# Optimization experiments

Hardware: AMD Instinct MI355X
Metric: run time of the kernel (lower is better)

## Reference

```python
import jax, jax.numpy as jnp
import numpy as np

DIM = 512
HEADS = 8
EPS = 1e-5


def layer_norm(x, g, b):
    mu = jnp.mean(x, axis=-1, keepdims=True)
    var = jnp.mean(jnp.square(x - mu), axis=-1, keepdims=True)
    return (x - mu) * jax.lax.rsqrt(var + EPS) * g + b


def setup_inputs() -> dict:
    key = jax.random.key(0)
    ks = jax.random.split(key, 8)
    d = DIM
    s = 0.02
    return {
        "x": jax.random.normal(ks[0], (2, d, 64, 64), jnp.float32),
        "ln1_g": jnp.ones((d,), jnp.float32),
        "ln1_b": jnp.zeros((d,), jnp.float32),
        "w_qkv": jax.random.normal(ks[1], (d, 3 * d), jnp.float32) * s,
        "b_qkv": jnp.zeros((3 * d,), jnp.float32),
        "w_proj": jax.random.normal(ks[2], (d, d), jnp.float32) * s,
        "b_proj": jnp.zeros((d,), jnp.float32),
        "ln2_g": jnp.ones((d,), jnp.float32),
        "ln2_b": jnp.zeros((d,), jnp.float32),
        "w_ffn1": jax.random.normal(ks[3], (d, 4 * d), jnp.float32) * s,
        "b_ffn1": jnp.zeros((4 * d,), jnp.float32),
        "w_ffn2": jax.random.normal(ks[4], (4 * d, d), jnp.float32) * s,
        "b_ffn2": jnp.zeros((d,), jnp.float32),
    }


def reference(x, ln1_g, ln1_b, w_qkv, b_qkv, w_proj, b_proj,
              ln2_g, ln2_b, w_ffn1, b_ffn1, w_ffn2, b_ffn2):
    B, C, H, W = x.shape
    hd = C // HEADS
    x_in = x
    t = x.reshape(B, C, H * W).transpose(0, 2, 1)  # [B, N, C]
    h = layer_norm(t, ln1_g, ln1_b)
    qkv = h @ w_qkv + b_qkv  # [B, N, 3C]
    q, k, v = jnp.split(qkv, 3, axis=-1)
    def to_heads(a):
        return a.reshape(B, -1, HEADS, hd).transpose(0, 2, 1, 3)  # [B, h, N, hd]
    q, k, v = to_heads(q), to_heads(k), to_heads(v)
    # NOTE: module scales by 1/sqrt(C), not 1/sqrt(head_dim)
    attn = jnp.einsum('bhqd,bhkd->bhqk', q, k) / jnp.sqrt(jnp.float32(C))
    attn = jax.nn.softmax(attn, axis=-1)
    out = jnp.einsum('bhqk,bhkd->bhqd', attn, v)
    out = out.transpose(0, 2, 1, 3).reshape(B, -1, C)
    out = out @ w_proj + b_proj
    t = t + out
    h2 = layer_norm(t, ln2_g, ln2_b)
    ffn = jax.nn.relu(h2 @ w_ffn1 + b_ffn1) @ w_ffn2 + b_ffn2
    t = t + ffn
    y = t.transpose(0, 2, 1).reshape(B, C, H, W)
    return y + x_in
```

## Files before the change

### kernel.cpp

```cpp
#include <hip/hip_runtime.h>
#include <hip/hip_bf16.h>

typedef __bf16 bf16;
typedef __bf16 bf16x8 __attribute__((ext_vector_type(8)));
typedef __bf16 bf16x4 __attribute__((ext_vector_type(4)));
typedef float f32x4 __attribute__((ext_vector_type(4)));
typedef int int4v __attribute__((ext_vector_type(4)));
typedef int int2v __attribute__((ext_vector_type(2)));

#define DEV static __device__ __forceinline__

DEV void gload16(const void* g, void* l) {
    __builtin_amdgcn_global_load_lds(
        (const __attribute__((address_space(1))) void*)g,
        (__attribute__((address_space(3))) void*)l, 16, 0, 0);
}

DEV f32x4 mfma16(bf16x8 a, bf16x8 b, f32x4 c) {
    return __builtin_amdgcn_mfma_f32_16x16x32_bf16(a, b, c, 0, 0, 0);
}

DEV int cvtpk(float lo, float hi) {
    int r;
    asm("v_cvt_pk_bf16_f32 %0, %1, %2" : "=v"(r) : "v"(lo), "v"(hi));
    return r;
}

DEV float rexp2(float x) {
    float r;
    asm("v_exp_f32 %0, %1" : "=v"(r) : "v"(x));
    return r;
}

__global__ __launch_bounds__(256)
void k_transpose_x(const float* __restrict__ x, float* __restrict__ t) {
    __shared__ float tile[32][33];
    int bid = blockIdx.x;
    int nt = bid & 127, ct = (bid >> 7) & 15, b = bid >> 11;
    int n0 = nt * 32, c0 = ct * 32;
    int tid = threadIdx.x;
    const float* xb = x + (size_t)b * 512 * 4096;
    int nl = tid & 31, cl = tid >> 5;
#pragma unroll
    for (int i = 0; i < 4; i++) {
        int c = cl + i * 8;
        tile[c][nl] = xb[(size_t)(c0 + c) * 4096 + n0 + nl];
    }
    __syncthreads();
    float* tb = t + (size_t)b * 4096 * 512;
    int cl2 = tid & 31, nl2 = tid >> 5;
#pragma unroll
    for (int i = 0; i < 4; i++) {
        int n = nl2 + i * 8;
        tb[(size_t)(n0 + n) * 512 + c0 + cl2] = tile[cl2][n];
    }
}

__global__ __launch_bounds__(256)
void k_out3(const float* __restrict__ t, const bf16* __restrict__ f2o,
            const float* __restrict__ x, float* __restrict__ y) {
    __shared__ float tile[32][33];
    int bid = blockIdx.x;
    int nt = bid & 127, ct = (bid >> 7) & 15, b = bid >> 11;
    int n0 = nt * 32, c0 = ct * 32;
    int tid = threadIdx.x;
#pragma unroll
    for (int i = 0; i < 4; i++) {
        int nl = (tid >> 5) + i * 8;
        size_t idx = (size_t)(b * 4096 + n0 + nl) * 512 + c0 + (tid & 31);
        tile[tid & 31][nl] = t[idx] + (float)f2o[idx];
    }
    __syncthreads();
    const float* xb = x + ((size_t)b * 512 + c0) * 4096;
    float* yb = y + ((size_t)b * 512 + c0) * 4096;
#pragma unroll
    for (int i = 0; i < 4; i++) {
        int cl = (tid >> 5) + i * 8;
        int nl = tid & 31;
        size_t off = (size_t)cl * 4096 + n0 + nl;
        yb[off] = tile[cl][nl] + xb[off];
    }
}

__global__ __launch_bounds__(256)
void k_ln(const float* __restrict__ t, const float* __restrict__ gg,
          const float* __restrict__ bb, bf16* __restrict__ h) {
    int lane = threadIdx.x & 63;
    int row = blockIdx.x * 4 + (threadIdx.x >> 6);
    const float* tr = t + (size_t)row * 512;
    f32x4 v0 = *(const f32x4*)(tr + lane * 4);
    f32x4 v1 = *(const f32x4*)(tr + 256 + lane * 4);
    float s = v0[0] + v0[1] + v0[2] + v0[3] + v1[0] + v1[1] + v1[2] + v1[3];
#pragma unroll
    for (int m = 1; m < 64; m <<= 1) s += __shfl_xor(s, m);
    float mu = s * (1.0f / 512.0f);
    float vs = 0.f;
#pragma unroll
    for (int j = 0; j < 4; j++) {
        float d0 = v0[j] - mu, d1 = v1[j] - mu;
        vs += d0 * d0 + d1 * d1;
    }
#pragma unroll
    for (int m = 1; m < 64; m <<= 1) vs += __shfl_xor(vs, m);
    float rs = rsqrtf(vs * (1.0f / 512.0f) + 1e-5f);
    f32x4 g0 = *(const f32x4*)(gg + lane * 4);
    f32x4 g1 = *(const f32x4*)(gg + 256 + lane * 4);
    f32x4 b0 = *(const f32x4*)(bb + lane * 4);
    f32x4 b1 = *(const f32x4*)(bb + 256 + lane * 4);
    bf16x4 o0, o1;
#pragma unroll
    for (int j = 0; j < 4; j++) {
        o0[j] = (bf16)((v0[j] - mu) * rs * g0[j] + b0[j]);
        o1[j] = (bf16)((v1[j] - mu) * rs * g1[j] + b1[j]);
    }
    *(bf16x4*)(h + (size_t)row * 512 + lane * 4) = o0;
    *(bf16x4*)(h + (size_t)row * 512 + 256 + lane * 4) = o1;
}

__global__ __launch_bounds__(256)
void k_lnr(float* __restrict__ t, const bf16* __restrict__ r,
           const float* __restrict__ gg, const float* __restrict__ bb,
           bf16* __restrict__ h) {
    int lane = threadIdx.x & 63;
    int row = blockIdx.x * 4 + (threadIdx.x >> 6);
    float* tr = t + (size_t)row * 512;
    f32x4 v0 = *(const f32x4*)(tr + lane * 4);
    f32x4 v1 = *(const f32x4*)(tr + 256 + lane * 4);
    bf16x4 r0 = *(const bf16x4*)(r + (size_t)row * 512 + lane * 4);
    bf16x4 r1 = *(const bf16x4*)(r + (size_t)row * 512 + 256 + lane * 4);
#pragma unroll
    for (int j = 0; j < 4; j++) {
        v0[j] += (float)r0[j];
        v1[j] += (float)r1[j];
    }
    *(f32x4*)(tr + lane * 4) = v0;
    *(f32x4*)(tr + 256 + lane * 4) = v1;
    float s = v0[0] + v0[1] + v0[2] + v0[3] + v1[0] + v1[1] + v1[2] + v1[3];
#pragma unroll
    for (int m = 1; m < 64; m <<= 1) s += __shfl_xor(s, m);
    float mu = s * (1.0f / 512.0f);
    float vs = 0.f;
#pragma unroll
    for (int j = 0; j < 4; j++) {
        float d0 = v0[j] - mu, d1 = v1[j] - mu;
        vs += d0 * d0 + d1 * d1;
    }
#pragma unroll
    for (int m = 1; m < 64; m <<= 1) vs += __shfl_xor(vs, m);
    float rs = rsqrtf(vs * (1.0f / 512.0f) + 1e-5f);
    f32x4 g0 = *(const f32x4*)(gg + lane * 4);
    f32x4 g1 = *(const f32x4*)(gg + 256 + lane * 4);
    f32x4 b0 = *(const f32x4*)(bb + lane * 4);
    f32x4 b1 = *(const f32x4*)(bb + 256 + lane * 4);
    bf16x4 o0, o1;
#pragma unroll
    for (int j = 0; j < 4; j++) {
        o0[j] = (bf16)((v0[j] - mu) * rs * g0[j] + b0[j]);
        o1[j] = (bf16)((v1[j] - mu) * rs * g1[j] + b1[j]);
    }
    *(bf16x4*)(h + (size_t)row * 512 + lane * 4) = o0;
    *(bf16x4*)(h + (size_t)row * 512 + 256 + lane * 4) = o1;
}

__global__ __launch_bounds__(256)
void k_wt(const float* __restrict__ w, bf16* __restrict__ wt, int K, int N) {
    __shared__ float tile[32][33];
    int ntn = N >> 5;
    int kt = blockIdx.x / ntn, ntile = blockIdx.x % ntn;
    int k0 = kt * 32, n0 = ntile * 32;
    int tid = threadIdx.x;
    int nl = tid & 31, kl = tid >> 5;
#pragma unroll
    for (int i = 0; i < 4; i++) {
        int k = kl + i * 8;
        tile[k][nl] = w[(size_t)(k0 + k) * N + n0 + nl];
    }
    __syncthreads();
    int kl2 = tid & 31, nl2 = tid >> 5;
#pragma unroll
    for (int i = 0; i < 4; i++) {
        int n = nl2 + i * 8;
        wt[(size_t)(n0 + n) * K + k0 + kl2] = (bf16)tile[kl2][n];
    }
}

template <int MODE, int BN>
__global__ __launch_bounds__(256, BN == 64 ? 3 : 2)
void k_gemm(const bf16* __restrict__ A, const bf16* __restrict__ BT,
            const float* __restrict__ bias, bf16* __restrict__ outb,
            bf16* __restrict__ vtout, int M, int N, int K) {
    constexpr int CG = BN / 32;
    constexpr int BSZ = CG * 4096;
    __shared__ char smem[32768 + 2 * BSZ];
    int ntn = N / BN;
    int nwg = gridDim.x;
    int bid = blockIdx.x;
    int cpx = nwg >> 3;
    bid = (bid & 7) * cpx + (bid >> 3);
    int bm = bid / ntn, bn = bid % ntn;
    int m0 = bm * 128, n0 = bn * BN;
    int tid = threadIdx.x;
    int w = tid >> 6, l = tid & 63;
    int wm = w >> 1, wn = w & 1;
    int l15 = l & 15, lg = l >> 4;

    f32x4 acc[4][CG];
#pragma unroll
    for (int i = 0; i < 4; i++)
#pragma unroll
        for (int j = 0; j < CG; j++) acc[i][j] = (f32x4){0.f, 0.f, 0.f, 0.f};

    int srow = tid >> 3, sphys = tid & 7;
    int lrow_a = wm * 64 + l15;
    int lrow_b = wn * (BN / 2) + l15;

#define GEMM_STAGE(k0v, bb)                                                  \
    do {                                                                     \
        _Pragma("unroll") for (int s = 0; s < 4; s++) {                      \
            int row = s * 32 + srow;                                         \
            int k16 = sphys ^ (row & 7);                                     \
            gload16(A + (size_t)(m0 + row) * K + (k0v) + k16 * 8,            \
                    smem + (bb) * 16384 + s * 4096 + tid * 16);              \
        }                                                                    \
        _Pragma("unroll") for (int s = 0; s < CG; s++) {                     \
            int row = s * 32 + srow;                                         \
            int k16 = sphys ^ (row & 7);                                     \
            gload16(BT + (size_t)(n0 + row) * K + (k0v) + k16 * 8,           \
                    smem + 32768 + (bb) * BSZ + s * 4096 + tid * 16);        \
        }                                                                    \
    } while (0)

    int nk = K >> 6;
    GEMM_STAGE(0, 0);
    int cur = 0;
    for (int kt = 0; kt < nk; kt++) {
        if (kt + 1 < nk) {
            GEMM_STAGE((kt + 1) << 6, cur ^ 1);
            if constexpr (BN == 128)
                asm volatile("s_waitcnt vmcnt(8)" ::: "memory");
            else
                asm volatile("s_waitcnt vmcnt(6)" ::: "memory");
        } else {
            asm volatile("s_waitcnt vmcnt(0)" ::: "memory");
        }
        __builtin_amdgcn_s_barrier();
        __builtin_amdgcn_sched_barrier(0);
        const char* pA = smem + cur * 16384;
        const char* pB = smem + 32768 + cur * BSZ;
#pragma unroll
        for (int ks = 0; ks < 2; ks++) {
            bf16x8 af[4], bfr[CG];
#pragma unroll
            for (int rg = 0; rg < 4; rg++) {
                int row = lrow_a + rg * 16;
                af[rg] = *(const bf16x8*)(pA + row * 128 +
                                          (((lg + ks * 4) ^ (row & 7)) << 4));
            }
#pragma unroll
            for (int cg = 0; cg < CG; cg++) {
                int row = lrow_b + cg * 16;
                bfr[cg] = *(const bf16x8*)(pB + row * 128 +
                                           (((lg + ks * 4) ^ (row & 7)) << 4));
            }
#pragma unroll
            for (int rg = 0; rg < 4; rg++)
#pragma unroll
                for (int cg = 0; cg < CG; cg++)
                    acc[rg][cg] = mfma16(af[rg], bfr[cg], acc[rg][cg]);
        }
        __builtin_amdgcn_s_barrier();
        cur ^= 1;
    }
#undef GEMM_STAGE

    if constexpr (MODE == 2) {
        if (n0 >= 1024) {
            char* vl = smem;
#pragma unroll
            for (int cg = 0; cg < CG; cg++) {
                int col = wn * 64 + cg * 16 + l15;
                float bz = bias[n0 + col];
#pragma unroll
                for (int rg = 0; rg < 4; rg++) {
                    int rowb = wm * 64 + rg * 16 + lg * 4;
                    int2v qq = {cvtpk(acc[rg][cg][0] + bz, acc[rg][cg][1] + bz),
                                cvtpk(acc[rg][cg][2] + bz, acc[rg][cg][3] + bz)};
                    *(int2v*)(vl + col * 272 + rowb * 2) = qq;
                }
            }
            __syncthreads();
            int b = m0 >> 12, nrow0 = m0 & 4095;
            int dl = tid >> 3, c8 = tid & 7;
#pragma unroll
            for (int dd = 0; dd < 4; dd++) {
                int d = dd * 32 + dl;
                int ch = (n0 - 1024) + d;
                bf16* dst = vtout +
                    ((size_t)((b * 8 + (ch >> 6)) * 64 + (ch & 63))) * 4096 + nrow0;
#pragma unroll
                for (int half = 0; half < 2; half++) {
                    int chunk = half * 8 + c8;
                    bf16x8 vv = *(const bf16x8*)(vl + d * 272 + chunk * 16);
                    *(bf16x8*)(dst + chunk * 8) = vv;
                }
            }
            return;
        }
    }

    constexpr int RS = BN * 2 + 8;
    constexpr int CH = BN / 8;
    char* ep = smem;
#pragma unroll
    for (int cg = 0; cg < CG; cg++) {
        int lcol = wn * (BN / 2) + cg * 16 + l15;
        float bz = bias[n0 + lcol];
#pragma unroll
        for (int rg = 0; rg < 4; rg++) {
#pragma unroll
            for (int j = 0; j < 4; j++) {
                int lrow = wm * 64 + rg * 16 + lg * 4 + j;
                float v = acc[rg][cg][j] + bz;
                if (MODE == 1) v = fmaxf(v, 0.f);
                *(bf16*)(ep + lrow * RS + lcol * 2) = (bf16)v;
            }
        }
    }
    __syncthreads();
    int cch = tid & (CH - 1);
    int rof = tid / CH;
    constexpr int RPP = 256 / CH;
#pragma unroll
    for (int i = 0; i < 128 / RPP; i++) {
        int row = i * RPP + rof;
        bf16x8 vv = *(const bf16x8*)(ep + row * RS + cch * 16);
        *(bf16x8*)(outb + (size_t)(m0 + row) * N + n0 + cch * 8) = vv;
    }
}

__global__ __launch_bounds__(256, 4)
void k_attn(const bf16* __restrict__ qkvb, const bf16* __restrict__ vt,
            bf16* __restrict__ attno) {
    __shared__ bf16 sK[2][64 * 64];
    __shared__ bf16 sV[2][64 * 64];
    const float sc = 0.044194173824159216f * 1.4426950408889634f;
    int bid = blockIdx.x;
    int nb = (bid & 7) * 128 + (bid >> 3);
    int bh = nb >> 6, qt = nb & 63;
    int b = bh >> 3, hh = bh & 7;
    int q0 = qt * 64;
    int tid = threadIdx.x, w = tid >> 6, l = tid & 63;
    int l15 = l & 15, lg = l >> 4, l7 = l15 & 7;
    int lg4 = lg * 4;
    int vperm = ((lg & 1) << 1) | (lg >> 1);
    const bf16* qbase = qkvb + (size_t)b * 4096 * 1536 + hh * 64;
    const bf16* kbase = qbase + 512;
    const bf16* vbase = vt + (size_t)bh * 64 * 4096;
    int srow = tid >> 3, sphys = tid & 7;

    const char* kp0 = (const char*)&sK[0][0] + l15 * 128 + ((lg ^ l7) << 4);
    const char* kp1 = (const char*)&sK[0][0] + l15 * 128 + (((4 + lg) ^ l7) << 4);
    const char* vp0 = (const char*)&sV[0][0] + l15 * 128 + ((vperm ^ l7) << 4);
    const char* vp1 = (const char*)&sV[0][0] + l15 * 128 + (((4 + vperm) ^ l7) << 4);
    char* dK0 = (char*)&sK[0][0] + tid * 16;
    char* dV0 = (char*)&sV[0][0] + tid * 16;
    const char* kg = (const char*)(kbase + srow * 1536 + (sphys ^ (srow & 7)) * 8);
    const char* vg = (const char*)(vbase + srow * 4096 + (sphys ^ (srow & 7)) * 8);

    gload16(kg, dK0);
    gload16(kg + 98304, dK0 + 4096);
    gload16(vg, dV0);
    gload16(vg + 262144, dV0 + 4096);
    kg += 196608;
    vg += 128;

    bf16x8 qf[2];
#pragma unroll
    for (int ks = 0; ks < 2; ks++) {
        bf16x8 v = *(const bf16x8*)(qbase +
            (size_t)(q0 + w * 16 + l15) * 1536 + ks * 32 + lg * 8);
        bf16x8 o;
#pragma unroll
        for (int j = 0; j < 8; j++) o[j] = (bf16)((float)v[j] * sc);
        qf[ks] = o;
    }

    const f32x4 kZ = {0.f, 0.f, 0.f, 0.f};
    float lsum = 0.f;
    f32x4 acc[4];
#pragma unroll
    for (int df = 0; df < 4; df++) acc[df] = kZ;

#define ABODY(BUF, PF)                                                        \
    {                                                                         \
        if (PF) {                                                             \
            gload16(kg, dK0 + (1 - (BUF)) * 8192);                            \
            gload16(kg + 98304, dK0 + (1 - (BUF)) * 8192 + 4096);             \
            gload16(vg, dV0 + (1 - (BUF)) * 8192);                            \
            gload16(vg + 262144, dV0 + (1 - (BUF)) * 8192 + 4096);            \
            kg += 196608;                                                     \
            vg += 128;                                                        \
            asm volatile("s_waitcnt vmcnt(4)" ::: "memory");                  \
        } else {                                                              \
            asm volatile("s_waitcnt vmcnt(0)" ::: "memory");                  \
        }                                                                     \
        __builtin_amdgcn_s_barrier();                                         \
        __builtin_amdgcn_sched_barrier(0);                                    \
        f32x4 s0, s1, s2, s3;                                                 \
        __builtin_amdgcn_s_setprio(1);                                        \
        s0 = mfma16(*(const bf16x8*)(kp0 + (BUF) * 8192 + 0 * 2048), qf[0], kZ); \
        s0 = mfma16(*(const bf16x8*)(kp1 + (BUF) * 8192 + 0 * 2048), qf[1], s0); \
        s1 = mfma16(*(const bf16x8*)(kp0 + (BUF) * 8192 + 1 * 2048), qf[0], kZ); \
        s1 = mfma16(*(const bf16x8*)(kp1 + (BUF) * 8192 + 1 * 2048), qf[1], s1); \
        __builtin_amdgcn_s_setprio(0);                                        \
        float e0 = rexp2(s0[0]), e1 = rexp2(s0[1]);                           \
        float e2 = rexp2(s0[2]), e3 = rexp2(s0[3]);                           \
        float e4 = rexp2(s1[0]), e5 = rexp2(s1[1]);                           \
        float e6 = rexp2(s1[2]), e7 = rexp2(s1[3]);                           \
        __builtin_amdgcn_s_setprio(1);                                        \
        s2 = mfma16(*(const bf16x8*)(kp0 + (BUF) * 8192 + 2 * 2048), qf[0], kZ); \
        s2 = mfma16(*(const bf16x8*)(kp1 + (BUF) * 8192 + 2 * 2048), qf[1], s2); \
        s3 = mfma16(*(const bf16x8*)(kp0 + (BUF) * 8192 + 3 * 2048), qf[0], kZ); \
        s3 = mfma16(*(const bf16x8*)(kp1 + (BUF) * 8192 + 3 * 2048), qf[1], s3); \
        __builtin_amdgcn_s_setprio(0);                                        \
        int p0 = cvtpk(e0, e1), p1 = cvtpk(e2, e3);                           \
        int p2 = cvtpk(e4, e5), p3 = cvtpk(e6, e7);                           \
        asm("v_permlane16_swap_b32 %0, %1" : "+v"(p2), "+v"(p0));             \
        asm("v_permlane16_swap_b32 %0, %1" : "+v"(p3), "+v"(p1));             \
        {                                                                     \
            int4v ai = {p0, p1, p2, p3};                                      \
            bf16x8 af = __builtin_bit_cast(bf16x8, ai);                       \
            __builtin_amdgcn_s_setprio(1);                                    \
            acc[0] = mfma16(af, *(const bf16x8*)(vp0 + (BUF) * 8192 + 0 * 2048), acc[0]); \
            acc[1] = mfma16(af, *(const bf16x8*)(vp0 + (BUF) * 8192 + 1 * 2048), acc[1]); \
            acc[2] = mfma16(af, *(const bf16x8*)(vp0 + (BUF) * 8192 + 2 * 2048), acc[2]); \
            acc[3] = mfma16(af, *(const bf16x8*)(vp0 + (BUF) * 8192 + 3 * 2048), acc[3]); \
            __builtin_amdgcn_s_setprio(0);                                    \
        }                                                                     \
        float e8 = rexp2(s2[0]), e9 = rexp2(s2[1]);                           \
        float e10 = rexp2(s2[2]), e11 = rexp2(s2[3]);                         \
        float e12 = rexp2(s3[0]), e13 = rexp2(s3[1]);                         \
        float e14 = rexp2(s3[2]), e15 = rexp2(s3[3]);                         \
        int p4 = cvtpk(e8, e9), p5 = cvtpk(e10, e11);                         \
        int p6 = cvtpk(e12, e13), p7 = cvtpk(e14, e15);                       \
        asm("v_permlane16_swap_b32 %0, %1" : "+v"(p6), "+v"(p4));             \
        asm("v_permlane16_swap_b32 %0, %1" : "+v"(p7), "+v"(p5));             \
        {                                                                     \
            int4v ai = {p4, p5, p6, p7};                                      \
            bf16x8 af = __builtin_bit_cast(bf16x8, ai);                       \
            __builtin_amdgcn_s_setprio(1);                                    \
            acc[0] = mfma16(af, *(const bf16x8*)(vp1 + (BUF) * 8192 + 0 * 2048), acc[0]); \
            acc[1] = mfma16(af, *(const bf16x8*)(vp1 + (BUF) * 8192 + 1 * 2048), acc[1]); \
            acc[2] = mfma16(af, *(const bf16x8*)(vp1 + (BUF) * 8192 + 2 * 2048), acc[2]); \
            acc[3] = mfma16(af, *(const bf16x8*)(vp1 + (BUF) * 8192 + 3 * 2048), acc[3]); \
            __builtin_amdgcn_s_setprio(0);                                    \
        }                                                                     \
        lsum += (((e0 + e1) + (e2 + e3)) + ((e4 + e5) + (e6 + e7))) +         \
                (((e8 + e9) + (e10 + e11)) + ((e12 + e13) + (e14 + e15)));    \
        __builtin_amdgcn_s_barrier();                                         \
    }

    for (int tt = 0; tt < 31; tt++) {
        ABODY(0, 1)
        ABODY(1, 1)
    }
    ABODY(0, 1)
    ABODY(1, 0)
#undef ABODY

    lsum += __shfl_xor(lsum, 16);
    lsum += __shfl_xor(lsum, 32);
    float invq[4];
#pragma unroll
    for (int j = 0; j < 4; j++)
        invq[j] = 1.0f / __shfl(lsum, lg4 + j);

    bf16* ow = (bf16*)&sK[0][0] + w * 16 * 64;
#pragma unroll
    for (int df = 0; df < 4; df++) {
        int chunk = df * 2 + (l15 >> 3);
        int within = l15 & 7;
#pragma unroll
        for (int j = 0; j < 4; j++) {
            int q = lg * 4 + j;
            *(bf16*)((char*)ow + q * 128 + ((chunk ^ (q & 7)) << 4) + within * 2) =
                (bf16)(acc[df][j] * invq[j]);
        }
    }
    __syncthreads();
    const char* owr = (const char*)ow;
#pragma unroll
    for (int half = 0; half < 2; half++) {
        int r = l >> 2, ch = (l & 3) + half * 4;
        bf16x8 vv = *(const bf16x8*)(owr + r * 128 + ((ch ^ (r & 7)) << 4));
        *(bf16x8*)(attno + (size_t)(b * 4096 + q0 + w * 16 + r) * 512 +
                   hh * 64 + ch * 8) = vv;
    }
}

extern "C" void kernel_launch(void* const* d_in, const int* in_sizes, int n_in,
                              void* d_out, int out_size, void* d_ws, size_t ws_size,
                              hipStream_t stream) {
    const float* x = (const float*)d_in[0];
    const float* ln1g = (const float*)d_in[1];
    const float* ln1b = (const float*)d_in[2];
    const float* wqkv = (const float*)d_in[3];
    const float* bqkv = (const float*)d_in[4];
    const float* wproj = (const float*)d_in[5];
    const float* bproj = (const float*)d_in[6];
    const float* ln2g = (const float*)d_in[7];
    const float* ln2b = (const float*)d_in[8];
    const float* wffn1 = (const float*)d_in[9];
    const float* bffn1 = (const float*)d_in[10];
    const float* wffn2 = (const float*)d_in[11];
    const float* bffn2 = (const float*)d_in[12];
    float* y = (float*)d_out;

    char* ws = (char*)d_ws;
    float* t    = (float*)(ws + 0);
    bf16* h     = (bf16*)(ws + 16777216);
    bf16* qkvb  = (bf16*)(ws + 25165824);
    bf16* vtb   = (bf16*)(ws + 50331648);
    bf16* f1    = (bf16*)(ws + 25165824);
    bf16* wqT   = (bf16*)(ws + 58720256);
    bf16* wpT   = (bf16*)(ws + 60293120);
    bf16* w1T   = (bf16*)(ws + 60817408);
    bf16* w2T   = (bf16*)(ws + 62914560);
    bf16* attno = h;
    bf16* po    = vtb;
    bf16* f2o   = h;

    k_transpose_x<<<4096, 256, 0, stream>>>(x, t);
    k_ln<<<2048, 256, 0, stream>>>(t, ln1g, ln1b, h);
    k_wt<<<(512 / 32) * (1536 / 32), 256, 0, stream>>>(wqkv, wqT, 512, 1536);
    k_wt<<<(512 / 32) * (512 / 32), 256, 0, stream>>>(wproj, wpT, 512, 512);
    k_wt<<<(512 / 32) * (2048 / 32), 256, 0, stream>>>(wffn1, w1T, 512, 2048);
    k_wt<<<(2048 / 32) * (512 / 32), 256, 0, stream>>>(wffn2, w2T, 2048, 512);

    k_gemm<2, 128><<<768, 256, 0, stream>>>(h, wqT, bqkv, qkvb, vtb, 8192, 1536, 512);
    k_attn<<<1024, 256, 0, stream>>>(qkvb, vtb, attno);
    k_gemm<0, 64><<<512, 256, 0, stream>>>(attno, wpT, bproj, po, nullptr, 8192, 512, 512);
    k_lnr<<<2048, 256, 0, stream>>>(t, po, ln2g, ln2b, h);
    k_gemm<1, 128><<<1024, 256, 0, stream>>>(h, w1T, bffn1, f1, nullptr, 8192, 2048, 512);
    k_gemm<0, 64><<<512, 256, 0, stream>>>(f1, w2T, bffn2, f2o, nullptr, 8192, 512, 2048);
    k_out3<<<4096, 256, 0, stream>>>(t, f2o, x, y);
}
```

Baseline: 201.2 us.

## Drop fp32 residual buffer, fuse transpose into layernorm, merge weight transposes

Result: no change. 204.0 us (+1.4%).

```diff
diff --git a/kernel.cpp b/kernel.cpp
--- a/kernel.cpp
+++ b/kernel.cpp
@@ -4,6 +4,7 @@
 typedef __bf16 bf16;
 typedef __bf16 bf16x8 __attribute__((ext_vector_type(8)));
 typedef __bf16 bf16x4 __attribute__((ext_vector_type(4)));
+typedef __bf16 bf16x2 __attribute__((ext_vector_type(2)));
 typedef float f32x4 __attribute__((ext_vector_type(4)));
 typedef int int4v __attribute__((ext_vector_type(4)));
 typedef int int2v __attribute__((ext_vector_type(2)));
@@ -32,141 +33,121 @@
     return r;
 }
 
-__global__ __launch_bounds__(256)
-void k_transpose_x(const float* __restrict__ x, float* __restrict__ t) {
+template <bool HASPO>
+__global__ __launch_bounds__(512)
+void k_tln(const float* __restrict__ x, const bf16* __restrict__ po,
+           const float* __restrict__ gg, const float* __restrict__ bb,
+           bf16* __restrict__ h) {
+    __shared__ bf16 big[32][520];
     __shared__ float tile[32][33];
     int bid = blockIdx.x;
-    int nt = bid & 127, ct = (bid >> 7) & 15, b = bid >> 11;
-    int n0 = nt * 32, c0 = ct * 32;
+    int nt = bid & 127, b = bid >> 7;
+    int n0 = nt * 32;
     int tid = threadIdx.x;
-    const float* xb = x + (size_t)b * 512 * 4096;
+    const float* xb = x + (size_t)b * 512 * 4096 + n0;
     int nl = tid & 31, cl = tid >> 5;
-#pragma unroll
-    for (int i = 0; i < 4; i++) {
-        int c = cl + i * 8;
-        tile[c][nl] = xb[(size_t)(c0 + c) * 4096 + n0 + nl];
+    int cl2 = tid & 31, nh = tid >> 5;
+    for (int ct = 0; ct < 16; ct++) {
+        int c0 = ct * 32;
+#pragma unroll
+        for (int i = 0; i < 2; i++) {
+            int c = cl + i * 16;
+            tile[c][nl] = xb[(size_t)(c0 + c) * 4096 + nl];
+        }
+        __syncthreads();
+#pragma unroll
+        for (int i = 0; i < 2; i++) {
+            int n = nh + i * 16;
+            big[n][c0 + cl2] = (bf16)tile[cl2][n];
+        }
+        __syncthreads();
+    }
+    int w = tid >> 6, l = tid & 63;
+    f32x4 g0 = *(const f32x4*)(gg + l * 8);
+    f32x4 g1 = *(const f32x4*)(gg + l * 8 + 4);
+    f32x4 bb0 = *(const f32x4*)(bb + l * 8);
+    f32x4 bb1 = *(const f32x4*)(bb + l * 8 + 4);
+#pragma unroll
+    for (int r = 0; r < 4; r++) {
+        int n = w * 4 + r;
+        bf16x8 vv = *(const bf16x8*)&big[n][l * 8];
+        float v[8];
+#pragma unroll
+        for (int j = 0; j < 8; j++) v[j] = (float)vv[j];
+        if (HASPO) {
+            bf16x8 pv = *(const bf16x8*)(po +
+                (size_t)(b * 4096 + n0 + n) * 512 + l * 8);
+#pragma unroll
+            for (int j = 0; j < 8; j++) v[j] += (float)pv[j];
+        }
+        float s = (((v[0] + v[1]) + (v[2] + v[3])) +
+                   ((v[4] + v[5]) + (v[6] + v[7])));
+#pragma unroll
+        for (int m = 1; m < 64; m <<= 1) s += __shfl_xor(s, m);
+        float mu = s * (1.0f / 512.0f);
+        float vs = 0.f;
+#pragma unroll
+        for (int j = 0; j < 8; j++) {
+            float d = v[j] - mu;
+            vs += d * d;
+        }
+#pragma unroll
+        for (int m = 1; m < 64; m <<= 1) vs += __shfl_xor(vs, m);
+        float rs = rsqrtf(vs * (1.0f / 512.0f) + 1e-5f);
+        bf16x8 o;
+#pragma unroll
+        for (int j = 0; j < 4; j++) {
+            o[j] = (bf16)((v[j] - mu) * rs * g0[j] + bb0[j]);
+            o[j + 4] = (bf16)((v[j + 4] - mu) * rs * g1[j] + bb1[j]);
+        }
+        *(bf16x8*)(h + (size_t)(b * 4096 + n0 + n) * 512 + l * 8) = o;
+    }
+}
+
+__global__ __launch_bounds__(256)
+void k_fin(const float* __restrict__ x, const bf16* __restrict__ po,
+           const bf16* __restrict__ f2o, float* __restrict__ y) {
+    __shared__ float ts[64][33];
+    int bid = blockIdx.x;
+    int nt = bid & 127, ct = (bid >> 7) & 7, b = bid >> 10;
+    int n0 = nt * 32, c0 = ct * 64;
+    int tid = threadIdx.x;
+    int pi = tid & 31, nr = tid >> 5;
+#pragma unroll
+    for (int p = 0; p < 4; p++) {
+        int n = nr + p * 8;
+        size_t ro = (size_t)(b * 4096 + n0 + n) * 512 + c0 + pi * 2;
+        bf16x2 pv = *(const bf16x2*)(po + ro);
+        bf16x2 fv = *(const bf16x2*)(f2o + ro);
+        ts[pi * 2][n] = (float)pv[0] + (float)fv[0];
+        ts[pi * 2 + 1][n] = (float)pv[1] + (float)fv[1];
     }
     __syncthreads();
-    float* tb = t + (size_t)b * 4096 * 512;
-    int cl2 = tid & 31, nl2 = tid >> 5;
-#pragma unroll
-    for (int i = 0; i < 4; i++) {
-        int n = nl2 + i * 8;
-        tb[(size_t)(n0 + n) * 512 + c0 + cl2] = tile[cl2][n];
+    int nw = tid & 31, cw = tid >> 5;
+#pragma unroll
+    for (int q = 0; q < 8; q++) {
+        int c = cw + q * 8;
+        size_t off = ((size_t)b * 512 + c0 + c) * 4096 + n0 + nw;
+        y[off] = 2.0f * x[off] + ts[c][nw];
     }
 }
 
 __global__ __launch_bounds__(256)
-void k_out3(const float* __restrict__ t, const bf16* __restrict__ f2o,
-            const float* __restrict__ x, float* __restrict__ y) {
+void k_wtall(const float* __restrict__ w0, const float* __restrict__ w1,
+             const float* __restrict__ w2, const float* __restrict__ w3,
+             bf16* __restrict__ d0, bf16* __restrict__ d1,
+             bf16* __restrict__ d2, bf16* __restrict__ d3) {
     __shared__ float tile[32][33];
     int bid = blockIdx.x;
-    int nt = bid & 127, ct = (bid >> 7) & 15, b = bid >> 11;
-    int n0 = nt * 32, c0 = ct * 32;
-    int tid = threadIdx.x;
-#pragma unroll
-    for (int i = 0; i < 4; i++) {
-        int nl = (tid >> 5) + i * 8;
-        size_t idx = (size_t)(b * 4096 + n0 + nl) * 512 + c0 + (tid & 31);
-        tile[tid & 31][nl] = t[idx] + (float)f2o[idx];
-    }
-    __syncthreads();
-    const float* xb = x + ((size_t)b * 512 + c0) * 4096;
-    float* yb = y + ((size_t)b * 512 + c0) * 4096;
-#pragma unroll
-    for (int i = 0; i < 4; i++) {
-        int cl = (tid >> 5) + i * 8;
-        int nl = tid & 31;
-        size_t off = (size_t)cl * 4096 + n0 + nl;
-        yb[off] = tile[cl][nl] + xb[off];
-    }
-}
-
-__global__ __launch_bounds__(256)
-void k_ln(const float* __restrict__ t, const float* __restrict__ gg,
-          const float* __restrict__ bb, bf16* __restrict__ h) {
-    int lane = threadIdx.x & 63;
-    int row = blockIdx.x * 4 + (threadIdx.x >> 6);
-    const float* tr = t + (size_t)row * 512;
-    f32x4 v0 = *(const f32x4*)(tr + lane * 4);
-    f32x4 v1 = *(const f32x4*)(tr + 256 + lane * 4);
-    float s = v0[0] + v0[1] + v0[2] + v0[3] + v1[0] + v1[1] + v1[2] + v1[3];
-#pragma unroll
-    for (int m = 1; m < 64; m <<= 1) s += __shfl_xor(s, m);
-    float mu = s * (1.0f / 512.0f);
-    float vs = 0.f;
-#pragma unroll
-    for (int j = 0; j < 4; j++) {
-        float d0 = v0[j] - mu, d1 = v1[j] - mu;
-        vs += d0 * d0 + d1 * d1;
-    }
-#pragma unroll
-    for (int m = 1; m < 64; m <<= 1) vs += __shfl_xor(vs, m);
-    float rs = rsqrtf(vs * (1.0f / 512.0f) + 1e-5f);
-    f32x4 g0 = *(const f32x4*)(gg + lane * 4);
-    f32x4 g1 = *(const f32x4*)(gg + 256 + lane * 4);
-    f32x4 b0 = *(const f32x4*)(bb + lane * 4);
-    f32x4 b1 = *(const f32x4*)(bb + 256 + lane * 4);
-    bf16x4 o0, o1;
-#pragma unroll
-    for (int j = 0; j < 4; j++) {
-        o0[j] = (bf16)((v0[j] - mu) * rs * g0[j] + b0[j]);
-        o1[j] = (bf16)((v1[j] - mu) * rs * g1[j] + b1[j]);
-    }
-    *(bf16x4*)(h + (size_t)row * 512 + lane * 4) = o0;
-    *(bf16x4*)(h + (size_t)row * 512 + 256 + lane * 4) = o1;
-}
-
-__global__ __launch_bounds__(256)
-void k_lnr(float* __restrict__ t, const bf16* __restrict__ r,
-           const float* __restrict__ gg, const float* __restrict__ bb,
-           bf16* __restrict__ h) {
-    int lane = threadIdx.x & 63;
-    int row = blockIdx.x * 4 + (threadIdx.x >> 6);
-    float* tr = t + (size_t)row * 512;
-    f32x4 v0 = *(const f32x4*)(tr + lane * 4);
-    f32x4 v1 = *(const f32x4*)(tr + 256 + lane * 4);
-    bf16x4 r0 = *(const bf16x4*)(r + (size_t)row * 512 + lane * 4);
-    bf16x4 r1 = *(const bf16x4*)(r + (size_t)row * 512 + 256 + lane * 4);
-#pragma unroll
-    for (int j = 0; j < 4; j++) {
-        v0[j] += (float)r0[j];
-        v1[j] += (float)r1[j];
-    }
-    *(f32x4*)(tr + lane * 4) = v0;
-    *(f32x4*)(tr + 256 + lane * 4) = v1;
-    float s = v0[0] + v0[1] + v0[2] + v0[3] + v1[0] + v1[1] + v1[2] + v1[3];
-#pragma unroll
-    for (int m = 1; m < 64; m <<= 1) s += __shfl_xor(s, m);
-    float mu = s * (1.0f / 512.0f);
-    float vs = 0.f;
-#pragma unroll
-    for (int j = 0; j < 4; j++) {
-        float d0 = v0[j] - mu, d1 = v1[j] - mu;
-        vs += d0 * d0 + d1 * d1;
-    }
-#pragma unroll
-    for (int m = 1; m < 64; m <<= 1) vs += __shfl_xor(vs, m);
-    float rs = rsqrtf(vs * (1.0f / 512.0f) + 1e-5f);
-    f32x4 g0 = *(const f32x4*)(gg + lane * 4);
-    f32x4 g1 = *(const f32x4*)(gg + 256 + lane * 4);
-    f32x4 b0 = *(const f32x4*)(bb + lane * 4);
-    f32x4 b1 = *(const f32x4*)(bb + 256 + lane * 4);
-    bf16x4 o0, o1;
-#pragma unroll
-    for (int j = 0; j < 4; j++) {
-        o0[j] = (bf16)((v0[j] - mu) * rs * g0[j] + b0[j]);
-        o1[j] = (bf16)((v1[j] - mu) * rs * g1[j] + b1[j]);
-    }
-    *(bf16x4*)(h + (size_t)row * 512 + lane * 4) = o0;
-    *(bf16x4*)(h + (size_t)row * 512 + 256 + lane * 4) = o1;
-}
-
-__global__ __launch_bounds__(256)
-void k_wt(const float* __restrict__ w, bf16* __restrict__ wt, int K, int N) {
-    __shared__ float tile[32][33];
+    const float* w;
+    bf16* d;
+    int K, N, t;
+    if (bid < 768)       { w = w0; d = d0; K = 512;  N = 1536; t = bid; }
+    else if (bid < 1024) { w = w1; d = d1; K = 512;  N = 512;  t = bid - 768; }
+    else if (bid < 2048) { w = w2; d = d2; K = 512;  N = 2048; t = bid - 1024; }
+    else                 { w = w3; d = d3; K = 2048; N = 512;  t = bid - 2048; }
     int ntn = N >> 5;
-    int kt = blockIdx.x / ntn, ntile = blockIdx.x % ntn;
+    int kt = t / ntn, ntile = t % ntn;
     int k0 = kt * 32, n0 = ntile * 32;
     int tid = threadIdx.x;
     int nl = tid & 31, kl = tid >> 5;
@@ -180,7 +161,7 @@
 #pragma unroll
     for (int i = 0; i < 4; i++) {
         int n = nl2 + i * 8;
-        wt[(size_t)(n0 + n) * K + k0 + kl2] = (bf16)tile[kl2][n];
+        d[(size_t)(n0 + n) * K + k0 + kl2] = (bf16)tile[kl2][n];
     }
 }
 
@@ -517,31 +498,30 @@
     float* y = (float*)d_out;
 
     char* ws = (char*)d_ws;
-    float* t    = (float*)(ws + 0);
-    bf16* h     = (bf16*)(ws + 16777216);
-    bf16* qkvb  = (bf16*)(ws + 25165824);
-    bf16* vtb   = (bf16*)(ws + 50331648);
-    bf16* f1    = (bf16*)(ws + 25165824);
-    bf16* wqT   = (bf16*)(ws + 58720256);
-    bf16* wpT   = (bf16*)(ws + 60293120);
-    bf16* w1T   = (bf16*)(ws + 60817408);
-    bf16* w2T   = (bf16*)(ws + 62914560);
+    bf16* po   = (bf16*)(ws + 0);
+    bf16* f2o  = (bf16*)(ws + 8388608);
+    bf16* h    = (bf16*)(ws + 16777216);
+    bf16* qkvb = (bf16*)(ws + 25165824);
+    bf16* vtb  = (bf16*)(ws + 50331648);
+    bf16* f1   = (bf16*)(ws + 25165824);
+    bf16* wqT  = (bf16*)(ws + 58720256);
+    bf16* wpT  = (bf16*)(ws + 60293120);
+    bf16* w1T  = (bf16*)(ws + 60817408);
+    bf16* w2T  = (bf16*)(ws + 62914560);
     bf16* attno = h;
-    bf16* po    = vtb;
-    bf16* f2o   = h;
-
-    k_transpose_x<<<4096, 256, 0, stream>>>(x, t);
-    k_ln<<<2048, 256, 0, stream>>>(t, ln1g, ln1b, h);
-    k_wt<<<(512 / 32) * (1536 / 32), 256, 0, stream>>>(wqkv, wqT, 512, 1536);
-    k_wt<<<(512 / 32) * (512 / 32), 256, 0, stream>>>(wproj, wpT, 512, 512);
-    k_wt<<<(512 / 32) * (2048 / 32), 256, 0, stream>>>(wffn1, w1T, 512, 2048);
-    k_wt<<<(2048 / 32) * (512 / 32), 256, 0, stream>>>(wffn2, w2T, 2048, 512);
-
-    k_gemm<2, 128><<<768, 256, 0, stream>>>(h, wqT, bqkv, qkvb, vtb, 8192, 1536, 512);
+
+    k_tln<false><<<256, 512, 0, stream>>>(x, nullptr, ln1g, ln1b, h);
+    k_wtall<<<3072, 256, 0, stream>>>(wqkv, wproj, wffn1, wffn2,
+                                      wqT, wpT, w1T, w2T);
+    k_gemm<2, 128><<<768, 256, 0, stream>>>(h, wqT, bqkv, qkvb, vtb,
+                                            8192, 1536, 512);
     k_attn<<<1024, 256, 0, stream>>>(qkvb, vtb, attno);
-    k_gemm<0, 64><<<512, 256, 0, stream>>>(attno, wpT, bproj, po, nullptr, 8192, 512, 512);
-    k_lnr<<<2048, 256, 0, stream>>>(t, po, ln2g, ln2b, h);
-    k_gemm<1, 128><<<1024, 256, 0, stream>>>(h, w1T, bffn1, f1, nullptr, 8192, 2048, 512);
-    k_gemm<0, 64><<<512, 256, 0, stream>>>(f1, w2T, bffn2, f2o, nullptr, 8192, 512, 2048);
-    k_out3<<<4096, 256, 0, stream>>>(t, f2o, x, y);
-}
+    k_gemm<0, 64><<<512, 256, 0, stream>>>(attno, wpT, bproj, po, nullptr,
+                                           8192, 512, 512);
+    k_tln<true><<<256, 512, 0, stream>>>(x, po, ln2g, ln2b, h);
+    k_gemm<1, 128><<<1024, 256, 0, stream>>>(h, w1T, bffn1, f1, nullptr,
+                                             8192, 2048, 512);
+    k_gemm<0, 64><<<512, 256, 0, stream>>>(f1, w2T, bffn2, f2o, nullptr,
+                                           8192, 512, 2048);
+    k_fin<<<2048, 256, 0, stream>>>(x, po, f2o, y);
+}
```
